# Performance work log

Hardware: AMD Instinct MI355X
Metric: run time of the kernel (lower is better)

## Reference

```python
import jax, jax.numpy as jnp
import numpy as np


def _build_schedule(N, M):
    """Round-robin (circle-method) tournament schedule of Givens rotations.

    Returns per-round, per-row arrays (R=N-1 rounds, each with N/2 disjoint pairs):
      partner[r, n]: row paired with n in round r (self if inactive)
      tpos[r, n]   : flat theta index for the pair (i<j: i*(N-1)-i*(i-1)/2 + j-i-1)
      sign[r, n]   : -1 for the lower-index row i, +1 for j, 0 if inactive
      active[r, n] : 1.0 if row participates in a rotation this round
    Pairs with min(i,j) >= M carry no theta and are skipped (identity).
    """
    assert N % 2 == 0, "even N assumed for the tournament schedule"
    R = N - 1
    players = list(range(N))
    partner = np.tile(np.arange(N, dtype=np.int32), (R, 1))
    tpos = np.zeros((R, N), np.int32)
    sign = np.zeros((R, N), np.float32)
    active = np.zeros((R, N), np.float32)
    for r in range(R):
        for k in range(N // 2):
            a, b = players[k], players[N - 1 - k]
            i, j = (a, b) if a < b else (b, a)
            if i >= M:
                continue
            t = i * (N - 1) - i * (i - 1) // 2 + (j - i - 1)
            partner[r, i], partner[r, j] = j, i
            tpos[r, i] = tpos[r, j] = t
            sign[r, i], sign[r, j] = -1.0, 1.0
            active[r, i] = active[r, j] = 1.0
        players = [players[0], players[-1]] + players[1:-1]
    return (jnp.asarray(partner), jnp.asarray(tpos),
            jnp.asarray(sign), jnp.asarray(active))


def _rotmat_forward(x, thetas, M=None):
    # x: [N, B]; applies the product of Givens rotations G(i,j,theta) round by round.
    N = x.shape[0]
    M = N if M is None else M
    sched = _build_schedule(N, M)

    def body(xc, rd):
        p, t, sg, ac = rd
        th = thetas[t]                       # [N]
        c = jnp.where(ac > 0, jnp.cos(th), 1.0)
        s = sg * jnp.sin(th)                 # 0 where inactive
        # row i: c*x[i] - s*x[j]; row j: s*x[i] + c*x[j]
        return c[:, None] * xc + s[:, None] * xc[p], None

    out, _ = jax.lax.scan(body, x, sched)
    return out


def setup_inputs() -> dict:
    key = jax.random.key(0)
    k1, k2 = jax.random.split(key)
    N, B = 512, 1024
    n_theta = N * (N - 1) // 2  # 130816 (M == N)
    x = jax.random.normal(k1, (N, B), dtype=jnp.float32)
    thetas = jax.random.normal(k2, (n_theta,), dtype=jnp.float32)
    return {"x": x, "thetas": thetas}


def reference(x, thetas):
    return _rotmat_forward(x, thetas)
```

## Files before the change

kernel.cpp:

```cpp
#include <hip/hip_runtime.h>
#include <hip/hip_fp16.h>


#define N_COLS   1024
#define PAIRS    256

typedef __attribute__((ext_vector_type(4))) float f32x4;

__global__ __launch_bounds__(256) void rotmat_setup(const float* __restrict__ thetas,
                                                    __half2* __restrict__ cs16) {
    const int r = blockIdx.x;
    const int k = threadIdx.x;
    int pu = (k == 0) ? 0 : ((k - 1 - r + 1022) % 511) + 1;
    int pv = ((510 - k - r + 1022) % 511) + 1;
    int i = min(pu, pv), j = max(pu, pv);
    int t = i * 511 - (i * (i - 1)) / 2 + (j - i - 1);
    float s, c;
    sincosf(thetas[t], &s, &c);
    float sp = (pu < pv) ? s : -s;
    cs16[r * 256 + k] = __floats2half2_rn(c, sp);
}

__device__ __forceinline__ float dpp_shr1(float old, float src) {
    return __int_as_float(__builtin_amdgcn_update_dpp(
        __float_as_int(old), __float_as_int(src), 0x138, 0xF, 0xF, false));
}
__device__ __forceinline__ float dpp_shl1(float old, float src) {
    return __int_as_float(__builtin_amdgcn_update_dpp(
        __float_as_int(old), __float_as_int(src), 0x130, 0xF, 0xF, false));
}

__device__ __forceinline__ void glds16(const void* g, void* l) {
    __builtin_amdgcn_global_load_lds(
        (const __attribute__((address_space(1))) void*)g,
        (__attribute__((address_space(3))) void*)l, 16, 0, 0);
}

__device__ __forceinline__ __half2 f2h2(float f) {
    union { float f; __half2 h; } u; u.f = f; return u.h;
}

#define ROUND(AA)                                                  \
    {                                                              \
        __half2 P0 = f2h2((AA).x), P3 = f2h2((AA).w);              \
        float c3 = __low2float(P3), s3 = __high2float(P3);         \
        float c0 = __low2float(P0), s0 = __high2float(P0);         \
        float t3 = s3 * hi[3], u3 = s3 * lo[3];                    \
        float l3 = fmaf(c3, lo[3], -t3);                           \
        float h3 = fmaf(c3, hi[3], u3);                            \
        float t0 = s0 * hi[0], u0 = s0 * lo[0];                    \
        float l0 = fmaf(c0, lo[0], -t0);                           \
        float h0 = fmaf(c0, hi[0], u0);                            \
        float nlo0 = dpp_shr1(l0, l3);                             \
        float nhi3 = dpp_shl1(l3, h0);                             \
        __half2 P1 = f2h2((AA).y), P2 = f2h2((AA).z);              \
        float c1 = __low2float(P1), s1 = __high2float(P1);         \
        float c2 = __low2float(P2), s2 = __high2float(P2);         \
        float t1 = s1 * hi[1], u1 = s1 * lo[1];                    \
        float l1 = fmaf(c1, lo[1], -t1);                           \
        float h1 = fmaf(c1, hi[1], u1);                            \
        float t2 = s2 * hi[2], u2 = s2 * lo[2];                    \
        float l2 = fmaf(c2, lo[2], -t2);                           \
        float h2 = fmaf(c2, hi[2], u2);                            \
        float nlo1 = is0 ? h0 : l0;                                \
        lo[0] = nlo0; lo[1] = nlo1; lo[2] = l1; lo[3] = l2;        \
        hi[0] = h1; hi[1] = h2; hi[2] = h3; hi[3] = nhi3;          \
    }

#define DSRD(dst, addr, imm)                                   \
    asm volatile("ds_read_b128 %0, %1 offset:%c2"              \
                 : "=v"(dst) : "v"(addr), "i"(imm))

#define WL3(a) asm volatile("s_waitcnt lgkmcnt(3)" : "+v"(a))
#define WL2(a) asm volatile("s_waitcnt lgkmcnt(2)" : "+v"(a))
#define WL1(a) asm volatile("s_waitcnt lgkmcnt(1)" : "+v"(a))
#define WL0(a) asm volatile("s_waitcnt lgkmcnt(0)" : "+v"(a))

#define WAITV(n) asm volatile("s_waitcnt vmcnt(" #n ")" ::: "memory")
#define BAR()                               \
    __builtin_amdgcn_s_barrier();           \
    __builtin_amdgcn_sched_barrier(0)

#define STAGE(cix, bix)                                              \
    {                                                                \
        const char* g_ = gsrc + (size_t)(cix)*16384;                 \
        char* l_ = lb + (size_t)(bix)*16384;                         \
        _Pragma("unroll")                                            \
        for (int j = 0; j < 4; ++j)                                  \
            glds16(g_ + j * 1024, l_ + j * 1024);                    \
    }

#define CHUNK16(ACUR, ANXT)                                    \
    WL3(A0); ROUND(A0) DSRD(A0, ACUR,  4 * 1024);              \
    WL3(A1); ROUND(A1) DSRD(A1, ACUR,  5 * 1024);              \
    WL3(A2); ROUND(A2) DSRD(A2, ACUR,  6 * 1024);              \
    WL3(A3); ROUND(A3) DSRD(A3, ACUR,  7 * 1024);              \
    WL3(A0); ROUND(A0) DSRD(A0, ACUR,  8 * 1024);              \
    WL3(A1); ROUND(A1) DSRD(A1, ACUR,  9 * 1024);              \
    WL3(A2); ROUND(A2) DSRD(A2, ACUR, 10 * 1024);              \
    WL3(A3); ROUND(A3) DSRD(A3, ACUR, 11 * 1024);              \
    WL3(A0); ROUND(A0) DSRD(A0, ACUR, 12 * 1024);              \
    WL3(A1); ROUND(A1) DSRD(A1, ACUR, 13 * 1024);              \
    WL3(A2); ROUND(A2) DSRD(A2, ACUR, 14 * 1024);              \
    WL3(A3); ROUND(A3) DSRD(A3, ACUR, 15 * 1024);              \
    WL3(A0); ROUND(A0) DSRD(A0, ANXT,  0 * 1024);              \
    WL3(A1); ROUND(A1) DSRD(A1, ANXT,  1 * 1024);              \
    WL3(A2); ROUND(A2) DSRD(A2, ANXT,  2 * 1024);              \
    WL3(A3); ROUND(A3) DSRD(A3, ANXT,  3 * 1024);

template <bool TAB>
__global__ __launch_bounds__(256, 1) void rotmat_main(const float* __restrict__ x,
                                                      const float* __restrict__ thetas,
                                                      const __half2* __restrict__ cs16,
                                                      float* __restrict__ out) {
    __shared__ f32x4 tab[3 * 1024];

    const int lane = threadIdx.x & 63;
    const int wave = threadIdx.x >> 6;
    const int col  = (blockIdx.x << 2) + wave;
    const int k0   = lane << 2;
    const bool is0 = (lane == 0);

    float lo[4], hi[4];
#pragma unroll
    for (int m = 0; m < 4; ++m) {
        lo[m] = x[(k0 + m) * N_COLS + col];
        hi[m] = x[(511 - k0 - m) * N_COLS + col];
    }

    if constexpr (TAB) {
        const char* gsrc = (const char*)cs16 + (size_t)wave * 4096 + (size_t)lane * 16;
        char* lb = (char*)(&tab[0]) + (size_t)wave * 4096;
        unsigned ldsLane;
        {
            auto p3 = (__attribute__((address_space(3))) char*)(&tab[0]);
            ldsLane = (unsigned)(size_t)p3 + (unsigned)(lane * 16);
        }

        f32x4 A0, A1, A2, A3;

        STAGE(0, 0)
        STAGE(1, 1)
        WAITV(0);
        BAR();
        {
            unsigned a0 = ldsLane;
            DSRD(A0, a0, 0 * 1024);
            DSRD(A1, a0, 1 * 1024);
            DSRD(A2, a0, 2 * 1024);
            DSRD(A3, a0, 3 * 1024);
        }

        int bufCur = 0, bufNxt = 1, bufStg = 2;
        for (int c = 0; c < 30; ++c) {
            WAITV(0);
            BAR();
            STAGE(c + 2, bufStg)
            unsigned aCur = ldsLane + (unsigned)bufCur * 16384u;
            unsigned aNxt = ldsLane + (unsigned)bufNxt * 16384u;
            CHUNK16(aCur, aNxt)
            int t_ = bufCur; bufCur = bufNxt; bufNxt = bufStg; bufStg = t_;
        }

        {
            WAITV(0);
            BAR();
            unsigned aCur = ldsLane + (unsigned)bufCur * 16384u;
            unsigned aNxt = ldsLane + (unsigned)bufNxt * 16384u;
            CHUNK16(aCur, aNxt)
            int t_ = bufCur; bufCur = bufNxt; bufNxt = bufStg; bufStg = t_;
        }

        {
            unsigned aCur = ldsLane + (unsigned)bufCur * 16384u;
            WL3(A0); ROUND(A0) DSRD(A0, aCur,  4 * 1024);
            WL3(A1); ROUND(A1) DSRD(A1, aCur,  5 * 1024);
            WL3(A2); ROUND(A2) DSRD(A2, aCur,  6 * 1024);
            WL3(A3); ROUND(A3) DSRD(A3, aCur,  7 * 1024);
            WL3(A0); ROUND(A0) DSRD(A0, aCur,  8 * 1024);
            WL3(A1); ROUND(A1) DSRD(A1, aCur,  9 * 1024);
            WL3(A2); ROUND(A2) DSRD(A2, aCur, 10 * 1024);
            WL3(A3); ROUND(A3) DSRD(A3, aCur, 11 * 1024);
            WL3(A0); ROUND(A0) DSRD(A0, aCur, 12 * 1024);
            WL3(A1); ROUND(A1) DSRD(A1, aCur, 13 * 1024);
            WL3(A2); ROUND(A2) DSRD(A2, aCur, 14 * 1024);
            WL3(A3); ROUND(A3)
            WL2(A0); ROUND(A0)
            WL1(A1); ROUND(A1)
            WL0(A2); ROUND(A2)
        }
    } else {
        int pu[4], pv[4];
#pragma unroll
        for (int m = 0; m < 4; ++m) {
            pu[m] = (k0 + m == 0) ? 0 : (k0 + m);
            pv[m] = 511 - (k0 + m);
        }
        for (int r = 0; r < 511; ++r) {
            float cc[4], ss[4];
#pragma unroll
            for (int m = 0; m < 4; ++m) {
                int i = min(pu[m], pv[m]), j = max(pu[m], pv[m]);
                int t = i * 511 - (i * (i - 1)) / 2 + (j - i - 1);
                float s, c;
                sincosf(thetas[t], &s, &c);
                cc[m] = c;
                ss[m] = (pu[m] < pv[m]) ? s : -s;
            }
            {
                float t3 = ss[3] * hi[3], u3 = ss[3] * lo[3];
                float l3 = fmaf(cc[3], lo[3], -t3);
                float h3 = fmaf(cc[3], hi[3], u3);
                float t0 = ss[0] * hi[0], u0 = ss[0] * lo[0];
                float l0 = fmaf(cc[0], lo[0], -t0);
                float h0 = fmaf(cc[0], hi[0], u0);
                float nlo0 = dpp_shr1(l0, l3);
                float nhi3 = dpp_shl1(l3, h0);
                float t1 = ss[1] * hi[1], u1 = ss[1] * lo[1];
                float l1 = fmaf(cc[1], lo[1], -t1);
                float h1 = fmaf(cc[1], hi[1], u1);
                float t2 = ss[2] * hi[2], u2 = ss[2] * lo[2];
                float l2 = fmaf(cc[2], lo[2], -t2);
                float h2 = fmaf(cc[2], hi[2], u2);
                float nlo1 = is0 ? h0 : l0;
                lo[0] = nlo0; lo[1] = nlo1; lo[2] = l1; lo[3] = l2;
                hi[0] = h1; hi[1] = h2; hi[2] = h3; hi[3] = nhi3;
            }
#pragma unroll
            for (int m = 0; m < 4; ++m) {
                pu[m] = (k0 + m == 0) ? 0 : ((pu[m] == 1) ? 511 : pu[m] - 1);
                pv[m] = (pv[m] == 1) ? 511 : pv[m] - 1;
            }
        }
    }

#pragma unroll
    for (int m = 0; m < 4; ++m) {
        out[(k0 + m) * N_COLS + col]       = lo[m];
        out[(511 - k0 - m) * N_COLS + col] = hi[m];
    }
}

extern "C" void kernel_launch(void* const* d_in, const int* in_sizes, int n_in,
                              void* d_out, int out_size, void* d_ws, size_t ws_size,
                              hipStream_t stream) {
    const float* x  = (const float*)d_in[0];
    const float* th = (const float*)d_in[1];
    float* out      = (float*)d_out;

    const size_t need = (size_t)512 * 1024;
    if (ws_size >= need) {
        __half2* cs16 = (__half2*)d_ws;
        rotmat_setup<<<511, PAIRS, 0, stream>>>(th, cs16);
        rotmat_main<true><<<N_COLS / 4, 256, 0, stream>>>(x, th, cs16, out);
    } else {
        rotmat_main<false><<<N_COLS / 4, 256, 0, stream>>>(x, th, nullptr, out);
    }
}
```

Measured before the change: 45.66 us.

## Process two columns per wave to amortize cos/sin table reads

Each wave now holds two adjacent columns in registers and applies every Givens round to both, so each LDS read of the cos/sin table serves twice the arithmetic. Blocks shrink to two waves (128 threads) and global loads and stores become float2. Each wave's staged table slice doubles to match. The idea is to halve LDS traffic and per-round overhead per column, at the cost of more registers per thread and only 512 waves in flight instead of 1024, which lowers occupancy and latency hiding.

```diff
diff --git a/kernel.cpp b/kernel.cpp
--- a/kernel.cpp
+++ b/kernel.cpp
@@ -40,31 +40,48 @@
     union { float f; __half2 h; } u; u.f = f; return u.h;
 }
 
-#define ROUND(AA)                                                  \
-    {                                                              \
-        __half2 P0 = f2h2((AA).x), P3 = f2h2((AA).w);              \
-        float c3 = __low2float(P3), s3 = __high2float(P3);         \
-        float c0 = __low2float(P0), s0 = __high2float(P0);         \
-        float t3 = s3 * hi[3], u3 = s3 * lo[3];                    \
-        float l3 = fmaf(c3, lo[3], -t3);                           \
-        float h3 = fmaf(c3, hi[3], u3);                            \
-        float t0 = s0 * hi[0], u0 = s0 * lo[0];                    \
-        float l0 = fmaf(c0, lo[0], -t0);                           \
-        float h0 = fmaf(c0, hi[0], u0);                            \
-        float nlo0 = dpp_shr1(l0, l3);                             \
-        float nhi3 = dpp_shl1(l3, h0);                             \
-        __half2 P1 = f2h2((AA).y), P2 = f2h2((AA).z);              \
-        float c1 = __low2float(P1), s1 = __high2float(P1);         \
-        float c2 = __low2float(P2), s2 = __high2float(P2);         \
-        float t1 = s1 * hi[1], u1 = s1 * lo[1];                    \
-        float l1 = fmaf(c1, lo[1], -t1);                           \
-        float h1 = fmaf(c1, hi[1], u1);                            \
-        float t2 = s2 * hi[2], u2 = s2 * lo[2];                    \
-        float l2 = fmaf(c2, lo[2], -t2);                           \
-        float h2 = fmaf(c2, hi[2], u2);                            \
-        float nlo1 = is0 ? h0 : l0;                                \
-        lo[0] = nlo0; lo[1] = nlo1; lo[2] = l1; lo[3] = l2;        \
-        hi[0] = h1; hi[1] = h2; hi[2] = h3; hi[3] = nhi3;          \
+#define ROUND2(AA)                                                    \
+    {                                                                 \
+        __half2 P0 = f2h2((AA).x), P1 = f2h2((AA).y);                 \
+        __half2 P2 = f2h2((AA).z), P3 = f2h2((AA).w);                 \
+        float c0 = __low2float(P0), s0 = __high2float(P0);            \
+        float c3 = __low2float(P3), s3 = __high2float(P3);            \
+        float t3a = s3 * hiA[3], u3a = s3 * loA[3];                   \
+        float l3a = fmaf(c3, loA[3], -t3a);                           \
+        float h3a = fmaf(c3, hiA[3], u3a);                            \
+        float t0a = s0 * hiA[0], u0a = s0 * loA[0];                   \
+        float l0a = fmaf(c0, loA[0], -t0a);                           \
+        float h0a = fmaf(c0, hiA[0], u0a);                            \
+        float t3b = s3 * hiB[3], u3b = s3 * loB[3];                   \
+        float l3b = fmaf(c3, loB[3], -t3b);                           \
+        float h3b = fmaf(c3, hiB[3], u3b);                            \
+        float t0b = s0 * hiB[0], u0b = s0 * loB[0];                   \
+        float l0b = fmaf(c0, loB[0], -t0b);                           \
+        float h0b = fmaf(c0, hiB[0], u0b);                            \
+        float nlo0a = dpp_shr1(l0a, l3a);                             \
+        float nhi3a = dpp_shl1(l3a, h0a);                             \
+        float nlo0b = dpp_shr1(l0b, l3b);                             \
+        float nhi3b = dpp_shl1(l3b, h0b);                             \
+        float c1 = __low2float(P1), s1 = __high2float(P1);            \
+        float c2 = __low2float(P2), s2 = __high2float(P2);            \
+        float t1a = s1 * hiA[1], u1a = s1 * loA[1];                   \
+        float l1a = fmaf(c1, loA[1], -t1a);                           \
+        float h1a = fmaf(c1, hiA[1], u1a);                            \
+        float t2a = s2 * hiA[2], u2a = s2 * loA[2];                   \
+        float l2a = fmaf(c2, loA[2], -t2a);                           \
+        float h2a = fmaf(c2, hiA[2], u2a);                            \
+        float t1b = s1 * hiB[1], u1b = s1 * loB[1];                   \
+        float l1b = fmaf(c1, loB[1], -t1b);                           \
+        float h1b = fmaf(c1, hiB[1], u1b);                            \
+        float t2b = s2 * hiB[2], u2b = s2 * loB[2];                   \
+        float l2b = fmaf(c2, loB[2], -t2b);                           \
+        float h2b = fmaf(c2, hiB[2], u2b);                            \
+        float nlo1a = is0 ? h0a : l0a;                                \
+        float nlo1b = is0 ? h0b : l0b;                                \
+        loA[0] = nlo0a; loA[1] = nlo1a; loA[2] = l1a; loA[3] = l2a;   \
+        hiA[0] = h1a; hiA[1] = h2a; hiA[2] = h3a; hiA[3] = nhi3a;     \
+        loB[0] = nlo0b; loB[1] = nlo1b; loB[2] = l1b; loB[3] = l2b;   \
+        hiB[0] = h1b; hiB[1] = h2b; hiB[2] = h3b; hiB[3] = nhi3b;     \
     }
 
 #define DSRD(dst, addr, imm)                                   \
@@ -86,30 +103,30 @@
         const char* g_ = gsrc + (size_t)(cix)*16384;                 \
         char* l_ = lb + (size_t)(bix)*16384;                         \
         _Pragma("unroll")                                            \
-        for (int j = 0; j < 4; ++j)                                  \
+        for (int j = 0; j < 8; ++j)                                  \
             glds16(g_ + j * 1024, l_ + j * 1024);                    \
     }
 
 #define CHUNK16(ACUR, ANXT)                                    \
-    WL3(A0); ROUND(A0) DSRD(A0, ACUR,  4 * 1024);              \
-    WL3(A1); ROUND(A1) DSRD(A1, ACUR,  5 * 1024);              \
-    WL3(A2); ROUND(A2) DSRD(A2, ACUR,  6 * 1024);              \
-    WL3(A3); ROUND(A3) DSRD(A3, ACUR,  7 * 1024);              \
-    WL3(A0); ROUND(A0) DSRD(A0, ACUR,  8 * 1024);              \
-    WL3(A1); ROUND(A1) DSRD(A1, ACUR,  9 * 1024);              \
-    WL3(A2); ROUND(A2) DSRD(A2, ACUR, 10 * 1024);              \
-    WL3(A3); ROUND(A3) DSRD(A3, ACUR, 11 * 1024);              \
-    WL3(A0); ROUND(A0) DSRD(A0, ACUR, 12 * 1024);              \
-    WL3(A1); ROUND(A1) DSRD(A1, ACUR, 13 * 1024);              \
-    WL3(A2); ROUND(A2) DSRD(A2, ACUR, 14 * 1024);              \
-    WL3(A3); ROUND(A3) DSRD(A3, ACUR, 15 * 1024);              \
-    WL3(A0); ROUND(A0) DSRD(A0, ANXT,  0 * 1024);              \
-    WL3(A1); ROUND(A1) DSRD(A1, ANXT,  1 * 1024);              \
-    WL3(A2); ROUND(A2) DSRD(A2, ANXT,  2 * 1024);              \
-    WL3(A3); ROUND(A3) DSRD(A3, ANXT,  3 * 1024);
+    WL3(A0); ROUND2(A0) DSRD(A0, ACUR,  4 * 1024);             \
+    WL3(A1); ROUND2(A1) DSRD(A1, ACUR,  5 * 1024);             \
+    WL3(A2); ROUND2(A2) DSRD(A2, ACUR,  6 * 1024);             \
+    WL3(A3); ROUND2(A3) DSRD(A3, ACUR,  7 * 1024);             \
+    WL3(A0); ROUND2(A0) DSRD(A0, ACUR,  8 * 1024);             \
+    WL3(A1); ROUND2(A1) DSRD(A1, ACUR,  9 * 1024);             \
+    WL3(A2); ROUND2(A2) DSRD(A2, ACUR, 10 * 1024);             \
+    WL3(A3); ROUND2(A3) DSRD(A3, ACUR, 11 * 1024);             \
+    WL3(A0); ROUND2(A0) DSRD(A0, ACUR, 12 * 1024);             \
+    WL3(A1); ROUND2(A1) DSRD(A1, ACUR, 13 * 1024);             \
+    WL3(A2); ROUND2(A2) DSRD(A2, ACUR, 14 * 1024);             \
+    WL3(A3); ROUND2(A3) DSRD(A3, ACUR, 15 * 1024);             \
+    WL3(A0); ROUND2(A0) DSRD(A0, ANXT,  0 * 1024);             \
+    WL3(A1); ROUND2(A1) DSRD(A1, ANXT,  1 * 1024);             \
+    WL3(A2); ROUND2(A2) DSRD(A2, ANXT,  2 * 1024);             \
+    WL3(A3); ROUND2(A3) DSRD(A3, ANXT,  3 * 1024);
 
 template <bool TAB>
-__global__ __launch_bounds__(256, 1) void rotmat_main(const float* __restrict__ x,
+__global__ __launch_bounds__(128, 1) void rotmat_main(const float* __restrict__ x,
                                                       const float* __restrict__ thetas,
                                                       const __half2* __restrict__ cs16,
                                                       float* __restrict__ out) {
@@ -117,20 +134,25 @@
 
     const int lane = threadIdx.x & 63;
     const int wave = threadIdx.x >> 6;
-    const int col  = (blockIdx.x << 2) + wave;
+    const int wid  = (blockIdx.x << 1) + wave;
     const int k0   = lane << 2;
     const bool is0 = (lane == 0);
 
-    float lo[4], hi[4];
+    const float2* x2  = reinterpret_cast<const float2*>(x);
+    float2* o2        = reinterpret_cast<float2*>(out);
+
+    float loA[4], hiA[4], loB[4], hiB[4];
 #pragma unroll
     for (int m = 0; m < 4; ++m) {
-        lo[m] = x[(k0 + m) * N_COLS + col];
-        hi[m] = x[(511 - k0 - m) * N_COLS + col];
+        float2 vlo = x2[(k0 + m) * 512 + wid];
+        float2 vhi = x2[(511 - k0 - m) * 512 + wid];
+        loA[m] = vlo.x; loB[m] = vlo.y;
+        hiA[m] = vhi.x; hiB[m] = vhi.y;
     }
 
     if constexpr (TAB) {
-        const char* gsrc = (const char*)cs16 + (size_t)wave * 4096 + (size_t)lane * 16;
-        char* lb = (char*)(&tab[0]) + (size_t)wave * 4096;
+        const char* gsrc = (const char*)cs16 + (size_t)wave * 8192 + (size_t)lane * 16;
+        char* lb = (char*)(&tab[0]) + (size_t)wave * 8192;
         unsigned ldsLane;
         {
             auto p3 = (__attribute__((address_space(3))) char*)(&tab[0]);
@@ -173,21 +195,21 @@
 
         {
             unsigned aCur = ldsLane + (unsigned)bufCur * 16384u;
-            WL3(A0); ROUND(A0) DSRD(A0, aCur,  4 * 1024);
-            WL3(A1); ROUND(A1) DSRD(A1, aCur,  5 * 1024);
-            WL3(A2); ROUND(A2) DSRD(A2, aCur,  6 * 1024);
-            WL3(A3); ROUND(A3) DSRD(A3, aCur,  7 * 1024);
-            WL3(A0); ROUND(A0) DSRD(A0, aCur,  8 * 1024);
-            WL3(A1); ROUND(A1) DSRD(A1, aCur,  9 * 1024);
-            WL3(A2); ROUND(A2) DSRD(A2, aCur, 10 * 1024);
-            WL3(A3); ROUND(A3) DSRD(A3, aCur, 11 * 1024);
-            WL3(A0); ROUND(A0) DSRD(A0, aCur, 12 * 1024);
-            WL3(A1); ROUND(A1) DSRD(A1, aCur, 13 * 1024);
-            WL3(A2); ROUND(A2) DSRD(A2, aCur, 14 * 1024);
-            WL3(A3); ROUND(A3)
-            WL2(A0); ROUND(A0)
-            WL1(A1); ROUND(A1)
-            WL0(A2); ROUND(A2)
+            WL3(A0); ROUND2(A0) DSRD(A0, aCur,  4 * 1024);
+            WL3(A1); ROUND2(A1) DSRD(A1, aCur,  5 * 1024);
+            WL3(A2); ROUND2(A2) DSRD(A2, aCur,  6 * 1024);
+            WL3(A3); ROUND2(A3) DSRD(A3, aCur,  7 * 1024);
+            WL3(A0); ROUND2(A0) DSRD(A0, aCur,  8 * 1024);
+            WL3(A1); ROUND2(A1) DSRD(A1, aCur,  9 * 1024);
+            WL3(A2); ROUND2(A2) DSRD(A2, aCur, 10 * 1024);
+            WL3(A3); ROUND2(A3) DSRD(A3, aCur, 11 * 1024);
+            WL3(A0); ROUND2(A0) DSRD(A0, aCur, 12 * 1024);
+            WL3(A1); ROUND2(A1) DSRD(A1, aCur, 13 * 1024);
+            WL3(A2); ROUND2(A2) DSRD(A2, aCur, 14 * 1024);
+            WL3(A3); ROUND2(A3)
+            WL2(A0); ROUND2(A0)
+            WL1(A1); ROUND2(A1)
+            WL0(A2); ROUND2(A2)
         }
     } else {
         int pu[4], pv[4];
@@ -207,7 +229,10 @@
                 cc[m] = c;
                 ss[m] = (pu[m] < pv[m]) ? s : -s;
             }
-            {
+#pragma unroll
+            for (int q = 0; q < 2; ++q) {
+                float* lo = q ? loB : loA;
+                float* hi = q ? hiB : hiA;
                 float t3 = ss[3] * hi[3], u3 = ss[3] * lo[3];
                 float l3 = fmaf(cc[3], lo[3], -t3);
                 float h3 = fmaf(cc[3], hi[3], u3);
@@ -236,8 +261,8 @@
 
 #pragma unroll
     for (int m = 0; m < 4; ++m) {
-        out[(k0 + m) * N_COLS + col]       = lo[m];
-        out[(511 - k0 - m) * N_COLS + col] = hi[m];
+        o2[(k0 + m) * 512 + wid]       = make_float2(loA[m], loB[m]);
+        o2[(511 - k0 - m) * 512 + wid] = make_float2(hiA[m], hiB[m]);
     }
 }
 
@@ -252,8 +277,8 @@
     if (ws_size >= need) {
         __half2* cs16 = (__half2*)d_ws;
         rotmat_setup<<<511, PAIRS, 0, stream>>>(th, cs16);
-        rotmat_main<true><<<N_COLS / 4, 256, 0, stream>>>(x, th, cs16, out);
+        rotmat_main<true><<<256, 128, 0, stream>>>(x, th, cs16, out);
     } else {
-        rotmat_main<false><<<N_COLS / 4, 256, 0, stream>>>(x, th, nullptr, out);
-    }
-}
+        rotmat_main<false><<<256, 128, 0, stream>>>(x, th, nullptr, out);
+    }
+}
```

Measured after the change: 53.91 us. 18.1% more time.
